# Kernel optimization log

Hardware: AMD Instinct MI355X
Metric: run time of the kernel (lower is better)

Reference implementation:

```python
import jax, jax.numpy as jnp
import numpy as np
from jax import lax


def get_grid(h, w):
    # normalized [-1,1] grid, channel 0 = x, channel 1 = y, shape [1,h,w,2]
    gx, gy = jnp.meshgrid(jnp.linspace(-1.0, 1.0, w), jnp.linspace(-1.0, 1.0, h))
    return jnp.stack([gx, gy], axis=-1)[None].astype(jnp.float32)


def gaussian_kernel(k, sigma=1.0):
    c = jnp.arange(k, dtype=jnp.float32) - (k - 1) / 2.0
    g = jnp.exp(-(c ** 2) / (2.0 * sigma ** 2))
    k2 = jnp.outer(g, g)
    return k2 / k2.sum()


def resize_bilinear(x, H, W):
    # x: [B,C,h,w]; torch F.interpolate(mode='bilinear', align_corners=False)
    B, C, h, w = x.shape
    def coords(n_out, n_in):
        c = (jnp.arange(n_out, dtype=jnp.float32) + 0.5) * (n_in / n_out) - 0.5
        c = jnp.clip(c, 0.0, n_in - 1.0)
        lo = jnp.floor(c).astype(jnp.int32)
        hi = jnp.minimum(lo + 1, n_in - 1)
        return lo, hi, c - lo.astype(jnp.float32)
    y0, y1, wy = coords(H, h)
    x0, x1, wx = coords(W, w)
    r = x[:, :, y0, :] * (1.0 - wy)[None, None, :, None] + x[:, :, y1, :] * wy[None, None, :, None]
    return r[:, :, :, x0] * (1.0 - wx) + r[:, :, :, x1] * wx


def _forward(src_grid, kernel, src_grid_base, tgt_grid, niter):
    B = src_grid.shape[0]
    H, W = tgt_grid.shape[1], tgt_grid.shape[2]
    ks = kernel.shape[-1]
    HW = H * W
    # forward displacement, resampled to target resolution, in pixel units
    dsrc = (src_grid - src_grid_base).transpose(0, 3, 1, 2)        # [B,2,Hs,Ws]
    dsrc = resize_bilinear(dsrc, H, W)                              # [B,2,H,W]
    dx = dsrc[:, 0].reshape(B, HW) * (W / 2.0)
    dy = dsrc[:, 1].reshape(B, HW) * (H / 2.0)
    xg = (jnp.arange(HW) % W).astype(jnp.float32)
    yg = (jnp.arange(HW) // W).astype(jnp.float32)
    xi = jnp.round(xg[None] + dx).astype(jnp.int32)
    yi = jnp.round(yg[None] + dy).astype(jnp.int32)
    oob = (xi < 0) | (yi < 0) | (xi > W - 1) | (yi > H - 1)
    field = jnp.where(oob, -1, yi * W + xi) + 1   # index 0 = trash slot
    # sort + dedup: duplicates are redirected to the trash slot
    order = jnp.argsort(field, axis=1)            # stable
    sf = jnp.take_along_axis(field, order, axis=1)
    keep = jnp.concatenate([jnp.ones((B, 1), bool), sf[:, 1:] != sf[:, :-1]], axis=1)
    sf = sf * keep
    inv_order = jnp.argsort(order, axis=1)
    field = jnp.take_along_axis(sf, inv_order, axis=1)
    # scatter inverse displacement (unique indices except trash slot 0)
    z = jnp.zeros((B, 1), dtype=dx.dtype)
    dxp = jnp.concatenate([z, dx], axis=1)
    dyp = jnp.concatenate([z, dy], axis=1)
    fieldp = jnp.concatenate([jnp.zeros((B, 1), field.dtype), field], axis=1)
    bidx = jnp.arange(B)[:, None]
    inv_dx = jnp.zeros_like(dxp).at[bidx, fieldp].set(-dxp)[:, 1:].reshape(B, H, W)
    inv_dy = jnp.zeros_like(dyp).at[bidx, fieldp].set(-dyp)[:, 1:].reshape(B, H, W)
    mask = (jnp.zeros_like(dxp).at[bidx, fieldp].set(1.0)[:, 1:].reshape(B, H, W)) > 0.5
    # pad so hole-fill never reads outside
    p = niter + 1
    inv_dx = jnp.pad(inv_dx, ((0, 0), (p, p), (p, p)))
    inv_dy = jnp.pad(inv_dy, ((0, 0), (p, p), (p, p)))
    mask = jnp.pad(mask, ((0, 0), (p, p), (p, p)))
    pd = ks // 2
    k4 = kernel.reshape(1, 1, ks, ks)
    def conv(x):
        return lax.conv_general_dilated(x[:, None], k4, (1, 1), [(pd, pd), (pd, pd)])[:, 0]
    # hole-fill: dilate mask by 4-neighborhood, fill with gaussian-weighted avg
    for _ in range(niter):
        nb = (jnp.pad(mask, ((0, 0), (1, 0), (0, 0)))[:, :-1]
              | jnp.pad(mask, ((0, 0), (0, 1), (0, 0)))[:, 1:]
              | jnp.pad(mask, ((0, 0), (0, 0), (1, 0)))[:, :, :-1]
              | jnp.pad(mask, ((0, 0), (0, 0), (0, 1)))[:, :, 1:])
        new_mask = (~mask) & nb
        new_dx = conv(inv_dx)
        new_dy = conv(inv_dy)
        new_sum = conv(mask.astype(inv_dx.dtype))
        denom = jnp.where(new_mask, new_sum, 1.0)  # safe: new_sum>0 where new_mask
        inv_dx = jnp.where(new_mask, new_dx / denom, inv_dx)
        inv_dy = jnp.where(new_mask, new_dy / denom, inv_dy)
        mask = mask | new_mask
    # erode: drop pixels with any unmasked 4-neighbor (outside counts as masked)
    for _ in range(niter):
        full = (jnp.pad(mask, ((0, 0), (1, 0), (0, 0)), constant_values=True)[:, :-1]
                & jnp.pad(mask, ((0, 0), (0, 1), (0, 0)), constant_values=True)[:, 1:]
                & jnp.pad(mask, ((0, 0), (0, 0), (1, 0)), constant_values=True)[:, :, :-1]
                & jnp.pad(mask, ((0, 0), (0, 0), (0, 1)), constant_values=True)[:, :, 1:])
        mask = mask & full
    inv_dx = jnp.where(mask, inv_dx, 2.0 * W)
    inv_dy = jnp.where(mask, inv_dy, 2.0 * H)
    inv_dx = inv_dx[:, p:-p, p:-p]
    inv_dy = inv_dy[:, p:-p, p:-p]
    dtgt = jnp.stack([inv_dx * (2.0 / W), inv_dy * (2.0 / H)], axis=3)
    return tgt_grid + dtgt


def setup_inputs() -> dict:
    key = jax.random.key(0)
    B, Hs, Ws, H, W = 8, 256, 256, 512, 512
    base = get_grid(Hs, Ws)
    src_grid = base + 0.05 * jax.random.normal(key, (B, Hs, Ws, 2), jnp.float32)
    return {
        "src_grid": src_grid,
        "kernel": gaussian_kernel(3),
        "src_grid_base": base,
        "tgt_grid": get_grid(H, W),
        "niter": 5,
    }


def reference(src_grid, kernel, src_grid_base, tgt_grid, niter):
    return _forward(src_grid, kernel, src_grid_base, tgt_grid, niter)
```

## Files before the change

### kernel.cpp

```cpp
#include <hip/hip_runtime.h>
#include <hip/hip_fp16.h>

typedef unsigned long long u64;
typedef unsigned int u32;
typedef float float4a __attribute__((ext_vector_type(4), aligned(4)));

#define B_    8
#define HS_   256
#define WS_   256
#define H_    512
#define W_    512
#define HW_   (H_ * W_)
#define TO_Y  16
#define NB    32
#define WR    36
#define COFF  6
#define KC    524
#define VSTR  528
#define INFW  0xFFFFFFFFu
#define CAPB  16384

__device__ __forceinline__ void bilin_disp(const float* __restrict__ src,
                                           const float* __restrict__ base,
                                           int b, int y, int x,
                                           float& dx, float& dy) {
#pragma clang fp contract(off)
    float cy = ((float)y + 0.5f) * 0.5f - 0.5f;
    cy = fminf(fmaxf(cy, 0.0f), 255.0f);
    int   y0 = (int)floorf(cy);
    int   y1 = min(y0 + 1, HS_ - 1);
    float wy = cy - (float)y0;

    float cx = ((float)x + 0.5f) * 0.5f - 0.5f;
    cx = fminf(fmaxf(cx, 0.0f), 255.0f);
    int   x0 = (int)floorf(cx);
    float wx = cx - (float)x0;

    float omy = 1.0f - wy;
    float wA, wB;
    int xs;
    if (x0 >= WS_ - 1) { xs = WS_ - 2; wA = 0.0f; wB = 1.0f; }
    else               { xs = x0;      wA = 1.0f - wx; wB = wx; }

    const float4a* S0 = (const float4a*)(src  + ((b * HS_ + y0) * WS_ + xs) * 2);
    const float4a* S1 = (const float4a*)(src  + ((b * HS_ + y1) * WS_ + xs) * 2);
    const float4a* B0 = (const float4a*)(base + (y0 * WS_ + xs) * 2);
    const float4a* B1 = (const float4a*)(base + (y1 * WS_ + xs) * 2);
    float4a s0 = *S0, s1 = *S1, b0 = *B0, b1 = *B1;

    float a00x = s0.x - b0.x, a00y = s0.y - b0.y;
    float a01x = s0.z - b0.z, a01y = s0.w - b0.w;
    float a10x = s1.x - b1.x, a10y = s1.y - b1.y;
    float a11x = s1.z - b1.z, a11y = s1.w - b1.w;

    float r0x = a00x * omy + a10x * wy;
    float r0y = a00y * omy + a10y * wy;
    float r1x = a01x * omy + a11x * wy;
    float r1y = a01y * omy + a11y * wy;
    dx = (r0x * wA + r1x * wB) * 256.0f;
    dy = (r0y * wA + r1y * wB) * 256.0f;
}

__device__ __forceinline__ u32 pack16(float x, float y) {
    __half hx = __float2half_rn(x), hy = __float2half_rn(y);
    return ((u32)__half_as_ushort(hy) << 16) | (u32)__half_as_ushort(hx);
}
__device__ __forceinline__ float2 unpack16(u32 p) {
    float2 f;
    f.x = __half2float(__ushort_as_half((unsigned short)(p & 0xFFFFu)));
    f.y = __half2float(__ushort_as_half((unsigned short)(p >> 16)));
    return f;
}

__device__ __forceinline__ u64 shfl_left(u64 v) {
    unsigned lo = __shfl_up((unsigned)v, 1);
    unsigned hi = __shfl_up((unsigned)(v >> 32), 1);
    u64 r = ((u64)hi << 32) | lo;
    return (threadIdx.x & 63) ? r : 0ull;
}
__device__ __forceinline__ u64 shfl_right(u64 v) {
    unsigned lo = __shfl_down((unsigned)v, 1);
    unsigned hi = __shfl_down((unsigned)(v >> 32), 1);
    u64 r = ((u64)hi << 32) | lo;
    return ((threadIdx.x & 63) == 63) ? 0ull : r;
}

__global__ void pre_k(const float* __restrict__ src,
                      const float* __restrict__ base,
                      u32* __restrict__ pay,
                      u32* __restrict__ gcount,
                      u32* __restrict__ bucket) {
    __shared__ u32 cnt[NB];
    __shared__ u32 bbase[NB];

    int bid = blockIdx.x;
    int b   = bid & 7;
    int t   = bid >> 3;
    int j   = t * 256 + threadIdx.x;
    int y   = j >> 9;
    int x   = j & (W_ - 1);

    if (threadIdx.x < NB) cnt[threadIdx.x] = 0;
    __syncthreads();

    float dx, dy;
    bilin_disp(src, base, b, y, x, dx, dy);
    pay[b * HW_ + j] = pack16(-dx, -dy);

    int xi = (int)rintf((float)x + dx);
    int yi = (int)rintf((float)y + dy);
    bool inb = (xi >= 0 && xi < W_ && yi >= 0 && yi < H_);
    int band = 0, rank = 0;
    if (inb) {
        band = yi >> 4;
        rank = atomicAdd(&cnt[band], 1u);
    }
    __syncthreads();
    if (threadIdx.x < NB && cnt[threadIdx.x] > 0)
        bbase[threadIdx.x] = atomicAdd(&gcount[b * NB + threadIdx.x],
                                       cnt[threadIdx.x]);
    __syncthreads();
    if (inb) {
        u32 slotn = bbase[band] + rank;
        if (slotn < CAPB) {
            u32 e = ((u32)(yi & 15) << 27) | ((u32)xi << 18) | (u32)j;
            bucket[(b * NB + band) * CAPB + slotn] = e;
        }
    }
}

__launch_bounds__(1024)
__global__ void fused3_k(const u32* __restrict__ pay,
                         const u32* __restrict__ gcount,
                         const u32* __restrict__ bucket,
                         const float* __restrict__ kern,
                         const float* __restrict__ tgt,
                         float* __restrict__ out) {
    __shared__ u32 key[WR * KC];
    __shared__ u32 val[WR * VSTR];

    int id   = blockIdx.x;
    int b    = id & 7;
    int tile = id >> 3;
    int Y0   = tile * TO_Y;
    int w0   = Y0 - 10;
    int tid  = threadIdx.x;

    float kw[9];
#pragma unroll
    for (int q = 0; q < 9; q++) kw[q] = kern[q];

    for (int i = tid; i < WR * KC; i += 1024) key[i] = INFW;
    for (int i = tid; i < WR * VSTR; i += 1024) val[i] = 0u;
    __syncthreads();

    for (int q = tile - 1; q <= tile + 1; q++) {
        if (q < 0 || q >= NB) continue;
        u32 cntq = min(gcount[b * NB + q], (u32)CAPB);
        const u32* bk = bucket + (b * NB + q) * CAPB;
        int ybase = q * TO_Y - w0;
        for (u32 i = tid; i < cntq; i += 1024) {
            u32 e  = bk[i];
            int wr = ybase + (int)((e >> 27) & 15u);
            if ((unsigned)wr < WR) {
                int xc = (int)((e >> 18) & 511u);
                atomicMin(&key[wr * KC + xc + COFF], e & 0x3FFFFu);
            }
        }
    }
    __syncthreads();

    {
        const u32* pb = pay + b * HW_;
        for (int idx = tid; idx < WR * KC; idx += 1024) {
            u32 k = key[idx];
            if (k != INFW) {
                int rr = idx / KC;
                int cc = idx - rr * KC;
                val[rr * VSTR + cc] = pb[k];
            }
        }
    }
    __syncthreads();

    int wv   = tid >> 6;
    int lane = tid & 63;
    int col  = 32 * wv - 16 + lane;
    int cls  = col + COFF;
    bool colin = (col >= -COFF) && (col <= W_ + 5);

    u64 m = 0;
    if (colin) {
#pragma unroll 6
        for (int r = 0; r < WR; r++)
            m |= (u64)(key[r * KC + cls] != INFW) << r;
    }

    int rlo = max(0, -COFF - w0);
    int rhi = min(WR - 1, (W_ + 5) - w0);
    u64 validm = colin ? ((((u64)1 << (rhi - rlo + 1)) - 1) << rlo) : 0ull;

    const u64 VROWS = (((u64)1 << 24) - 1) << 6;
    bool vlane = (lane >= 6 && lane <= 57);

    for (int it = 0; it < 5; it++) {
        u64 mL = shfl_left(m), mR = shfl_right(m);
        u64 cand = ~m & ((m << 1) | (m >> 1) | mL | mR) & validm;
        u64 cv = vlane ? (cand & VROWS) : 0ull;
        while (cv) {
            int r = __builtin_ctzll(cv);
            cv &= cv - 1;
            float s = 0.0f, ax = 0.0f, ay = 0.0f;
#pragma unroll
            for (int dr = -1; dr <= 1; dr++) {
#pragma unroll
                for (int dc = -1; dc <= 1; dc++) {
                    if (dr == 0 && dc == 0) continue;
                    u64 nm = (dc < 0) ? mL : ((dc > 0) ? mR : m);
                    float wq = ((nm >> (r + dr)) & 1)
                                 ? kw[(dr + 1) * 3 + (dc + 1)] : 0.0f;
                    int cc = min(max(cls + dc, 0), KC - 1);
                    float2 nv = unpack16(val[(r + dr) * VSTR + cc]);
                    s += wq; ax += wq * nv.x; ay += wq * nv.y;
                }
            }
            val[r * VSTR + cls] = pack16(ax / s, ay / s);
        }
        m |= cand;
        __syncthreads();
    }

    for (int it = 0; it < 5; it++) {
        u64 mL = shfl_left(m), mR = shfl_right(m);
        m &= (m << 1) & (m >> 1) & mL & mR;
    }

    if (lane >= 16 && lane < 48) {
#pragma unroll 4
        for (int r = 10; r < 10 + TO_Y; r++) {
            int row = w0 + r;
            bool on = (m >> r) & 1;
            float vx, vy;
            if (on) {
                float2 t = unpack16(val[r * VSTR + cls]);
                vx = t.x * (1.0f / 256.0f);
                vy = t.y * (1.0f / 256.0f);
            } else {
                vx = 4.0f; vy = 4.0f;
            }
            int ti = (row * W_ + col) * 2;
            float2 tg = *(const float2*)(tgt + ti);
            float2 ov; ov.x = tg.x + vx; ov.y = tg.y + vy;
            ((float2*)out)[(size_t)b * HW_ + row * W_ + col] = ov;
        }
    }
}

extern "C" void kernel_launch(void* const* d_in, const int* in_sizes, int n_in,
                              void* d_out, int out_size, void* d_ws, size_t ws_size,
                              hipStream_t stream) {
    const float* src  = (const float*)d_in[0];
    const float* kern = (const float*)d_in[1];
    const float* base = (const float*)d_in[2];
    const float* tgt  = (const float*)d_in[3];
    float* out = (float*)d_out;

    char* ws = (char*)d_ws;
    u32* gcount = (u32*)ws;
    u32* pay    = (u32*)(ws + 1024);
    u32* bucket = (u32*)(ws + 1024 + (size_t)B_ * HW_ * 4);

    hipMemsetAsync(gcount, 0, B_ * NB * sizeof(u32), stream);

    pre_k<<<(B_ * HW_) / 256, 256, 0, stream>>>(src, base, pay, gcount, bucket);
    fused3_k<<<256, 1024, 0, stream>>>(pay, gcount, bucket, kern, tgt, out);
}
```

Measured before the change: 145.1 us.

## Merge key/value LDS planes, halve output tile height, enlarge pre-pass blocks

The fused kernel now keeps a single shared plane: it scatters min-indices into it, extracts the occupancy mask, and then overwrites each entry in place with the gathered payload. This removes the separate key array and cuts LDS use per block. Output tiles shrink from 16 to 8 rows, doubling the grid to 512 blocks, which should allow more blocks per CU at the cost of a larger halo fraction and more redundant bucket reads. The pre-pass uses 1024-thread blocks, so there are fewer per-block global atomics, and the division in the smoothing loop becomes a hardware reciprocal, which is slightly less exact.

```diff
diff --git a/kernel.cpp b/kernel.cpp
--- a/kernel.cpp
+++ b/kernel.cpp
@@ -11,12 +11,14 @@
 #define H_    512
 #define W_    512
 #define HW_   (H_ * W_)
-#define TO_Y  16
+#define TO_Y  8
+#define NTY   64
+#define BND   16
 #define NB    32
-#define WR    36
+#define WR    28
 #define COFF  6
-#define KC    524
-#define VSTR  528
+#define PC    524
+#define VSTR  531
 #define INFW  0xFFFFFFFFu
 #define CAPB  16384
 
@@ -85,6 +87,7 @@
     return ((threadIdx.x & 63) == 63) ? 0ull : r;
 }
 
+__launch_bounds__(1024)
 __global__ void pre_k(const float* __restrict__ src,
                       const float* __restrict__ base,
                       u32* __restrict__ pay,
@@ -96,7 +99,7 @@
     int bid = blockIdx.x;
     int b   = bid & 7;
     int t   = bid >> 3;
-    int j   = t * 256 + threadIdx.x;
+    int j   = t * 1024 + threadIdx.x;
     int y   = j >> 9;
     int x   = j & (W_ - 1);
 
@@ -129,15 +132,14 @@
     }
 }
 
-__launch_bounds__(1024)
-__global__ void fused3_k(const u32* __restrict__ pay,
+__launch_bounds__(1024, 8)
+__global__ void fused4_k(const u32* __restrict__ pay,
                          const u32* __restrict__ gcount,
                          const u32* __restrict__ bucket,
                          const float* __restrict__ kern,
                          const float* __restrict__ tgt,
                          float* __restrict__ out) {
-    __shared__ u32 key[WR * KC];
-    __shared__ u32 val[WR * VSTR];
+    __shared__ u32 plane[WR * VSTR];
 
     int id   = blockIdx.x;
     int b    = id & 7;
@@ -150,34 +152,23 @@
 #pragma unroll
     for (int q = 0; q < 9; q++) kw[q] = kern[q];
 
-    for (int i = tid; i < WR * KC; i += 1024) key[i] = INFW;
-    for (int i = tid; i < WR * VSTR; i += 1024) val[i] = 0u;
-    __syncthreads();
-
-    for (int q = tile - 1; q <= tile + 1; q++) {
-        if (q < 0 || q >= NB) continue;
-        u32 cntq = min(gcount[b * NB + q], (u32)CAPB);
-        const u32* bk = bucket + (b * NB + q) * CAPB;
-        int ybase = q * TO_Y - w0;
-        for (u32 i = tid; i < cntq; i += 1024) {
-            u32 e  = bk[i];
-            int wr = ybase + (int)((e >> 27) & 15u);
-            if ((unsigned)wr < WR) {
-                int xc = (int)((e >> 18) & 511u);
-                atomicMin(&key[wr * KC + xc + COFF], e & 0x3FFFFu);
-            }
-        }
-    }
+    for (int i = tid; i < WR * VSTR; i += 1024) plane[i] = INFW;
     __syncthreads();
 
     {
-        const u32* pb = pay + b * HW_;
-        for (int idx = tid; idx < WR * KC; idx += 1024) {
-            u32 k = key[idx];
-            if (k != INFW) {
-                int rr = idx / KC;
-                int cc = idx - rr * KC;
-                val[rr * VSTR + cc] = pb[k];
+        int qlo = max(0, w0 >> 4);
+        int qhi = min(NB - 1, (w0 + WR - 1) >> 4);
+        for (int q = qlo; q <= qhi; q++) {
+            u32 cntq = min(gcount[b * NB + q], (u32)CAPB);
+            const u32* bk = bucket + (b * NB + q) * CAPB;
+            int ybase = q * BND - w0;
+            for (u32 i = tid; i < cntq; i += 1024) {
+                u32 e  = bk[i];
+                int wr = ybase + (int)((e >> 27) & 15u);
+                if ((unsigned)wr < WR) {
+                    int xc = (int)((e >> 18) & 511u);
+                    atomicMin(&plane[wr * VSTR + xc + COFF], e & 0x3FFFFu);
+                }
             }
         }
     }
@@ -191,16 +182,29 @@
 
     u64 m = 0;
     if (colin) {
-#pragma unroll 6
+#pragma unroll 7
         for (int r = 0; r < WR; r++)
-            m |= (u64)(key[r * KC + cls] != INFW) << r;
-    }
+            m |= (u64)(plane[r * VSTR + cls] != INFW) << r;
+    }
+    __syncthreads();
+
+    {
+        const u32* pb = pay + b * HW_;
+        for (int idx = tid; idx < WR * PC; idx += 1024) {
+            int rr = idx / PC;
+            int cc = idx - rr * PC;
+            int off = rr * VSTR + cc;
+            u32 k = plane[off];
+            plane[off] = (k != INFW) ? pb[k] : 0u;
+        }
+    }
+    __syncthreads();
 
     int rlo = max(0, -COFF - w0);
     int rhi = min(WR - 1, (W_ + 5) - w0);
     u64 validm = colin ? ((((u64)1 << (rhi - rlo + 1)) - 1) << rlo) : 0ull;
 
-    const u64 VROWS = (((u64)1 << 24) - 1) << 6;
+    const u64 VROWS = (((u64)1 << 16) - 1) << 6;
     bool vlane = (lane >= 6 && lane <= 57);
 
     for (int it = 0; it < 5; it++) {
@@ -219,12 +223,13 @@
                     u64 nm = (dc < 0) ? mL : ((dc > 0) ? mR : m);
                     float wq = ((nm >> (r + dr)) & 1)
                                  ? kw[(dr + 1) * 3 + (dc + 1)] : 0.0f;
-                    int cc = min(max(cls + dc, 0), KC - 1);
-                    float2 nv = unpack16(val[(r + dr) * VSTR + cc]);
+                    int cc = min(max(cls + dc, 0), PC - 1);
+                    float2 nv = unpack16(plane[(r + dr) * VSTR + cc]);
                     s += wq; ax += wq * nv.x; ay += wq * nv.y;
                 }
             }
-            val[r * VSTR + cls] = pack16(ax / s, ay / s);
+            float rs = __builtin_amdgcn_rcpf(s);
+            plane[r * VSTR + cls] = pack16(ax * rs, ay * rs);
         }
         m |= cand;
         __syncthreads();
@@ -242,7 +247,7 @@
             bool on = (m >> r) & 1;
             float vx, vy;
             if (on) {
-                float2 t = unpack16(val[r * VSTR + cls]);
+                float2 t = unpack16(plane[r * VSTR + cls]);
                 vx = t.x * (1.0f / 256.0f);
                 vy = t.y * (1.0f / 256.0f);
             } else {
@@ -272,6 +277,6 @@
 
     hipMemsetAsync(gcount, 0, B_ * NB * sizeof(u32), stream);
 
-    pre_k<<<(B_ * HW_) / 256, 256, 0, stream>>>(src, base, pay, gcount, bucket);
-    fused3_k<<<256, 1024, 0, stream>>>(pay, gcount, bucket, kern, tgt, out);
-}
+    pre_k<<<(B_ * HW_) / 1024, 1024, 0, stream>>>(src, base, pay, gcount, bucket);
+    fused4_k<<<512, 1024, 0, stream>>>(pay, gcount, bucket, kern, tgt, out);
+}
```

After: 139.7 us. 1.04x faster.
